# Performance work log

Measured on AMD Instinct MI355X. Metric: run time of the kernel, lower is better.

## Reference

```python
import jax, jax.numpy as jnp
import numpy as np

IN_F = 4096
OUT_F = 4096
N = 16384


def setup_inputs() -> dict:
    key = jax.random.key(0)
    kx, kw = jax.random.split(key)
    x = jax.random.normal(kx, (N, IN_F), dtype=jnp.float32)
    # reset_parameters: weight ~ N(0, 1/in_features), bias = 0
    weight = jax.random.normal(kw, (OUT_F, IN_F), dtype=jnp.float32) * (1.0 / np.sqrt(IN_F))
    bias = jnp.zeros((OUT_F,), dtype=jnp.float32)
    return {"x": x, "weight": weight, "bias": bias}


def reference(x, weight, bias):
    # binary_linear_scalar: per-output-row scaling factor alpha = mean(|W|),
    # binarized weight bw = sign(W) * alpha  (XNOR-Net style)
    alpha = jnp.mean(jnp.abs(weight), axis=1, keepdims=True)  # [out, 1]
    bw = jnp.sign(weight) * alpha                             # [out, in]
    # y = x @ bw^T + bias
    return jnp.einsum('ni,oi->no', x, bw) + bias
```

## Files before the change

### kernel.cpp

```cpp
#include <hip/hip_runtime.h>
#include <hip/hip_bf16.h>
#include <stdint.h>

#define IN_F  4096
#define OUT_F 4096
#define NROWS 16384
#define NT    (IN_F / 64)

typedef unsigned short u16;
typedef unsigned int u32;
typedef unsigned long long u64;
typedef __bf16 bf16x8 __attribute__((ext_vector_type(8)));
typedef float  f32x4  __attribute__((ext_vector_type(4)));
typedef u16    u16x8  __attribute__((ext_vector_type(8)));

#define BAR()   asm volatile("s_barrier" ::: "memory")
#define LGKM0() asm volatile("s_waitcnt lgkmcnt(0)" ::: "memory")
#define VM4()   asm volatile("s_waitcnt vmcnt(4)" ::: "memory")
#define VM0()   asm volatile("s_waitcnt vmcnt(0)" ::: "memory")

__device__ __forceinline__ u16 f2bf(float x) {
    union { float f; uint32_t u; } c; c.f = x;
    uint32_t u = c.u;
    return (u16)((u + 0x7FFFu + ((u >> 16) & 1u)) >> 16);
}

__device__ __forceinline__ void gload_lds16(const void* g, void* l) {
    __builtin_amdgcn_global_load_lds(
        (const __attribute__((address_space(1))) void*)g,
        (__attribute__((address_space(3))) void*)l, 16, 0, 0);
}

__device__ __forceinline__ u16 sgn_bf16(float v) {
    return v > 0.f ? 0x3F80 : (v < 0.f ? 0xBF80 : 0);
}

__global__ void prep_wbits_kernel(const float* __restrict__ W,
                                  float* __restrict__ alpha,
                                  u64* __restrict__ Wbits) {
    const int row = blockIdx.x;
    const int wave = threadIdx.x >> 6, lane = threadIdx.x & 63;
    const float* wr = W + (size_t)row * IN_F;
    float s = 0.f;
#pragma unroll 4
    for (int it = 0; it < 16; ++it) {
        const int kword = it * 4 + wave;
        float v = __builtin_nontemporal_load(wr + kword * 64 + lane);
        s += fabsf(v);
        u64 m = __ballot(v > 0.f);
        if (lane == 0) Wbits[(size_t)kword * OUT_F + row] = m;
    }
    for (int off = 32; off > 0; off >>= 1) s += __shfl_down(s, off);
    __shared__ float red[4];
    if (lane == 0) red[wave] = s;
    __syncthreads();
    if (threadIdx.x == 0)
        alpha[row] = (red[0] + red[1] + red[2] + red[3]) * (1.0f / IN_F);
}

__global__ void convx_kernel(const float* __restrict__ X, u16* __restrict__ O,
                             int swz) {
    const size_t idx = (size_t)blockIdx.x * 256 + threadIdx.x;
    const int row = (int)(idx >> 9);
    const int q = (int)idx & 511;
    const int g = q >> 3, c8 = q & 7;
    const int c8s = swz ? (c8 ^ (row & 7)) : c8;
    const f32x4* src = reinterpret_cast<const f32x4*>(
        X + (size_t)row * IN_F + g * 64 + c8s * 8);
    f32x4 a = __builtin_nontemporal_load(src);
    f32x4 b = __builtin_nontemporal_load(src + 1);
    u16x8 r;
    r[0] = f2bf(a[0]); r[1] = f2bf(a[1]); r[2] = f2bf(a[2]); r[3] = f2bf(a[3]);
    r[4] = f2bf(b[0]); r[5] = f2bf(b[1]); r[6] = f2bf(b[2]); r[7] = f2bf(b[3]);
    reinterpret_cast<u16x8*>(O)[idx] = r;
}

__global__ __launch_bounds__(512, 2) void gemm8_kernel(
    const u16* __restrict__ Xbf, const u64* __restrict__ Wbits,
    const float* __restrict__ alpha, const float* __restrict__ bias,
    float* __restrict__ Y) {
    __shared__ u16 Alds[3][16384];
    __shared__ u16 Blds[2][16384];

    const int tid  = threadIdx.x;
    const int lane = tid & 63, wave = tid >> 6;
    const int wm = wave >> 2, wn = wave & 3;
    const int lrow = lane & 15;

    const int wg = blockIdx.x;
    const int i  = wg >> 3;
    const int m0 = (((wg & 7) << 3) | (i >> 4)) << 8;
    const int n0 = (i & 15) << 8;

    const int q0 = ((lane >> 4) << 3) ^ ((lrow & 7) << 3);
    const int q1 = q0 ^ 32;

    const int erow = tid >> 1, ehalf = tid & 1;
    const u32* Wb32 = reinterpret_cast<const u32*>(Wbits);

    f32x4 acc[8][4];
#pragma unroll
    for (int a = 0; a < 8; ++a)
#pragma unroll
        for (int b = 0; b < 4; ++b) acc[a][b] = (f32x4){0.f, 0.f, 0.f, 0.f};

    auto stageA = [&](int th, int half, u16* buf) {
        if (th >= NT) return;
#pragma unroll
        for (int t2 = 0; t2 < 2; ++t2) {
            const int c = half * 1024 + t2 * 512 + tid;
            const int row = c >> 3, c8 = c & 7;
            gload_lds16(Xbf + (size_t)(m0 + row) * IN_F + th * 64 + c8 * 8,
                        buf + c * 8);
        }
    };

    auto expandB = [&](unsigned b, int dstbuf, int jlo) {
        unsigned nb = ~b;
        u16* base = &Blds[dstbuf][erow * 64];
#pragma unroll
        for (int j = 0; j < 2; ++j) {
            const int jj = jlo + j;
            const int k8 = 4 * ehalf + jj;
            union { unsigned u[4]; u16x8 v; } r;
#pragma unroll
            for (int e = 0; e < 4; ++e) {
                unsigned s = nb >> (jj * 8 + 2 * e);
                r.u[e] = 0x3F803F80u | ((s & 1u) << 15) | ((s & 2u) << 30);
            }
            *reinterpret_cast<u16x8*>(base + ((k8 ^ (erow & 7)) << 3)) = r.v;
        }
    };

    u16* pa0 = &Alds[0][0];
    u16* pa1 = &Alds[1][0];
    u16* pa2 = &Alds[2][0];

    unsigned b0 = Wb32[(size_t)(n0 + erow) * 2 + ehalf];
    stageA(0, 0, pa0); stageA(0, 1, pa0);
    unsigned bits_cur = Wb32[(size_t)8192 + (n0 + erow) * 2 + ehalf];
    stageA(1, 0, pa1); stageA(1, 1, pa1);
    unsigned bits_nxt = 0;
    expandB(b0, 0, 0); expandB(b0, 0, 2);
    VM4();
    LGKM0(); BAR();

    for (int t = 0; t < NT; ++t) {
        const u16* Ar = pa0 + wm * 8192 + lrow * 64;
        const u16* Br = &Blds[t & 1][0] + wn * 4096 + lrow * 64;
        bf16x8 a0[4][2], a1[4][2], bfr[4][2];

#pragma unroll
        for (int mm = 0; mm < 4; ++mm) {
            a0[mm][0] = *reinterpret_cast<const bf16x8*>(Ar + mm * 1024 + q0);
            a0[mm][1] = *reinterpret_cast<const bf16x8*>(Ar + mm * 1024 + q1);
        }
#pragma unroll
        for (int nf = 0; nf < 4; ++nf) {
            bfr[nf][0] = *reinterpret_cast<const bf16x8*>(Br + nf * 1024 + q0);
            bfr[nf][1] = *reinterpret_cast<const bf16x8*>(Br + nf * 1024 + q1);
        }
#pragma unroll
        for (int mm = 0; mm < 4; ++mm) {
            a1[mm][0] = *reinterpret_cast<const bf16x8*>(Ar + (4 + mm) * 1024 + q0);
            a1[mm][1] = *reinterpret_cast<const bf16x8*>(Ar + (4 + mm) * 1024 + q1);
        }
        if (t + 2 < NT)
            bits_nxt = Wb32[(size_t)(t + 2) * 8192 + (n0 + erow) * 2 + ehalf];

        __builtin_amdgcn_s_setprio(1);
#pragma unroll
        for (int mm = 0; mm < 4; ++mm)
#pragma unroll
            for (int nn = 0; nn < 4; ++nn) {
                acc[mm][nn] = __builtin_amdgcn_mfma_f32_16x16x32_bf16(a0[mm][0], bfr[nn][0], acc[mm][nn], 0, 0, 0);
                acc[mm][nn] = __builtin_amdgcn_mfma_f32_16x16x32_bf16(a0[mm][1], bfr[nn][1], acc[mm][nn], 0, 0, 0);
            }
        __builtin_amdgcn_s_setprio(0);

        stageA(t + 2, 0, pa2);
        stageA(t + 2, 1, pa2);
        if (t + 1 < NT) {
            expandB(bits_cur, (t + 1) & 1, 0);
            expandB(bits_cur, (t + 1) & 1, 2);
        }

        __builtin_amdgcn_s_setprio(1);
#pragma unroll
        for (int mm = 0; mm < 4; ++mm)
#pragma unroll
            for (int nn = 0; nn < 4; ++nn) {
                acc[4 + mm][nn] = __builtin_amdgcn_mfma_f32_16x16x32_bf16(a1[mm][0], bfr[nn][0], acc[4 + mm][nn], 0, 0, 0);
                acc[4 + mm][nn] = __builtin_amdgcn_mfma_f32_16x16x32_bf16(a1[mm][1], bfr[nn][1], acc[4 + mm][nn], 0, 0, 0);
            }
        __builtin_amdgcn_s_setprio(0);

        if (t >= NT - 2) { VM0(); } else { VM4(); }
        LGKM0(); BAR();

        bits_cur = bits_nxt;
        u16* tp = pa0; pa0 = pa1; pa1 = pa2; pa2 = tp;
    }

#pragma unroll
    for (int nf = 0; nf < 4; ++nf) {
        const int col = n0 + wn * 64 + nf * 16 + lrow;
        const float al = alpha[col], bi = bias[col];
#pragma unroll
        for (int mf = 0; mf < 8; ++mf) {
            const int rbase = m0 + wm * 128 + mf * 16 + ((lane >> 4) << 2);
#pragma unroll
            for (int r = 0; r < 4; ++r)
                __builtin_nontemporal_store(acc[mf][nf][r] * al + bi,
                    &Y[(size_t)(rbase + r) * OUT_F + col]);
        }
    }
}

__global__ void prep_w_kernel(const float* __restrict__ W,
                              float* __restrict__ alpha,
                              u16* __restrict__ S) {
    const int row = blockIdx.x;
    const float* wr = W + (size_t)row * IN_F;
    float s = 0.f;
    for (int c = threadIdx.x; c < 512; c += 256) {
        const f32x4* src = reinterpret_cast<const f32x4*>(wr + c * 8);
        f32x4 v0 = __builtin_nontemporal_load(src);
        f32x4 v1 = __builtin_nontemporal_load(src + 1);
        s += fabsf(v0[0]) + fabsf(v0[1]) + fabsf(v0[2]) + fabsf(v0[3])
           + fabsf(v1[0]) + fabsf(v1[1]) + fabsf(v1[2]) + fabsf(v1[3]);
        u16x8 r;
        r[0] = sgn_bf16(v0[0]); r[1] = sgn_bf16(v0[1]);
        r[2] = sgn_bf16(v0[2]); r[3] = sgn_bf16(v0[3]);
        r[4] = sgn_bf16(v1[0]); r[5] = sgn_bf16(v1[1]);
        r[6] = sgn_bf16(v1[2]); r[7] = sgn_bf16(v1[3]);
        *reinterpret_cast<u16x8*>(S + (size_t)row * IN_F + c * 8) = r;
    }
    for (int off = 32; off > 0; off >>= 1) s += __shfl_down(s, off);
    __shared__ float red[4];
    const int wave = threadIdx.x >> 6, lane = threadIdx.x & 63;
    if (lane == 0) red[wave] = s;
    __syncthreads();
    if (threadIdx.x == 0)
        alpha[row] = (red[0] + red[1] + red[2] + red[3]) * (1.0f / IN_F);
}

__global__ __launch_bounds__(256) void gemm_fallback(
    const float* __restrict__ X, const u16* __restrict__ Wsign,
    const float* __restrict__ alpha, const float* __restrict__ bias,
    float* __restrict__ Y) {
    __shared__ u16 Axl[128 * 64];
    __shared__ u16 Bxl[128 * 64];

    const int tid = threadIdx.x;
    const int n0 = blockIdx.x * 128;
    const int m0 = blockIdx.y * 128;
    const int wave = tid >> 6, lane = tid & 63;
    const int wm = wave >> 1, wn = wave & 1;
    const int lrow = lane & 15;
    const int lk8 = (lane >> 4) * 8;

    f32x4 acc[4][4];
#pragma unroll
    for (int a = 0; a < 4; ++a)
#pragma unroll
        for (int b = 0; b < 4; ++b) acc[a][b] = (f32x4){0.f, 0.f, 0.f, 0.f};

    for (int kt = 0; kt < IN_F; kt += 64) {
#pragma unroll
        for (int j = 0; j < 4; ++j) {
            const int idx = j * 256 + tid;
            const int row = idx >> 3, c8 = idx & 7;
            gload_lds16(Wsign + (size_t)(n0 + row) * IN_F + kt + c8 * 8,
                        &Bxl[idx * 8]);
        }
#pragma unroll
        for (int j = 0; j < 4; ++j) {
            const int idx = j * 256 + tid;
            const int row = idx >> 3, c8 = idx & 7;
            const float* src = X + (size_t)(m0 + row) * IN_F + kt + c8 * 8;
            float4 v0 = *reinterpret_cast<const float4*>(src);
            float4 v1 = *reinterpret_cast<const float4*>(src + 4);
            u16x8 r;
            r[0] = f2bf(v0.x); r[1] = f2bf(v0.y); r[2] = f2bf(v0.z); r[3] = f2bf(v0.w);
            r[4] = f2bf(v1.x); r[5] = f2bf(v1.y); r[6] = f2bf(v1.z); r[7] = f2bf(v1.w);
            *reinterpret_cast<u16x8*>(&Axl[idx * 8]) = r;
        }
        __syncthreads();
#pragma unroll
        for (int kk = 0; kk < 2; ++kk) {
            bf16x8 af[4], bfv[4];
#pragma unroll
            for (int mf = 0; mf < 4; ++mf)
                af[mf] = *reinterpret_cast<const bf16x8*>(
                    &Axl[(wm * 64 + mf * 16 + lrow) * 64 + kk * 32 + lk8]);
#pragma unroll
            for (int nf = 0; nf < 4; ++nf)
                bfv[nf] = *reinterpret_cast<const bf16x8*>(
                    &Bxl[(wn * 64 + nf * 16 + lrow) * 64 + kk * 32 + lk8]);
#pragma unroll
            for (int mf = 0; mf < 4; ++mf)
#pragma unroll
                for (int nf = 0; nf < 4; ++nf)
                    acc[mf][nf] = __builtin_amdgcn_mfma_f32_16x16x32_bf16(
                        af[mf], bfv[nf], acc[mf][nf], 0, 0, 0);
        }
        __syncthreads();
    }
#pragma unroll
    for (int nf = 0; nf < 4; ++nf) {
        const int col = n0 + wn * 64 + nf * 16 + lrow;
        const float al = alpha[col], bi = bias[col];
#pragma unroll
        for (int mf = 0; mf < 4; ++mf) {
            const int rbase = m0 + wm * 64 + mf * 16 + (lane >> 4) * 4;
#pragma unroll
            for (int r = 0; r < 4; ++r)
                __builtin_nontemporal_store(acc[mf][nf][r] * al + bi,
                    &Y[(size_t)(rbase + r) * OUT_F + col]);
        }
    }
}

extern "C" void kernel_launch(void* const* d_in, const int* in_sizes, int n_in,
                              void* d_out, int out_size, void* d_ws, size_t ws_size,
                              hipStream_t stream) {
    const float* X    = (const float*)d_in[0];
    const float* W    = (const float*)d_in[1];
    const float* bias = (const float*)d_in[2];
    float* Y = (float*)d_out;

    char* ws = (char*)d_ws;
    float* alpha = (float*)ws;
    const size_t WBITS_OFF = 16384;
    const size_t XBF_OFF   = WBITS_OFF + (size_t)OUT_F * (IN_F / 8);
    const size_t need_fast = XBF_OFF + (size_t)NROWS * IN_F * 2;

    if (ws_size >= need_fast) {
        u64* Wbits = (u64*)(ws + WBITS_OFF);
        u16* Xbf   = (u16*)(ws + XBF_OFF);
        prep_wbits_kernel<<<OUT_F, 256, 0, stream>>>(W, alpha, Wbits);
        convx_kernel<<<(size_t)NROWS * IN_F / 8 / 256, 256, 0, stream>>>(X, Xbf, 1);
        gemm8_kernel<<<dim3(1024), 512, 0, stream>>>(Xbf, Wbits, alpha, bias, Y);
    } else {
        u16* Wsign = (u16*)(ws + 16384);
        prep_w_kernel<<<OUT_F, 256, 0, stream>>>(W, alpha, Wsign);
        dim3 grid(OUT_F / 128, NROWS / 128);
        gemm_fallback<<<grid, 256, 0, stream>>>(X, Wsign, alpha, bias, Y);
    }
}
```

Baseline: 523.5 us.

## Software-pipeline A fragment LDS loads and interleave staging with MFMA blocks

Result: no change. 514.3 us (-1.8%).

```diff
diff --git a/kernel.cpp b/kernel.cpp
--- a/kernel.cpp
+++ b/kernel.cpp
@@ -148,52 +148,39 @@
     for (int t = 0; t < NT; ++t) {
         const u16* Ar = pa0 + wm * 8192 + lrow * 64;
         const u16* Br = &Blds[t & 1][0] + wn * 4096 + lrow * 64;
-        bf16x8 a0[4][2], a1[4][2], bfr[4][2];
-
-#pragma unroll
-        for (int mm = 0; mm < 4; ++mm) {
-            a0[mm][0] = *reinterpret_cast<const bf16x8*>(Ar + mm * 1024 + q0);
-            a0[mm][1] = *reinterpret_cast<const bf16x8*>(Ar + mm * 1024 + q1);
-        }
+        bf16x8 bfr[4][2];
+
 #pragma unroll
         for (int nf = 0; nf < 4; ++nf) {
             bfr[nf][0] = *reinterpret_cast<const bf16x8*>(Br + nf * 1024 + q0);
             bfr[nf][1] = *reinterpret_cast<const bf16x8*>(Br + nf * 1024 + q1);
         }
-#pragma unroll
-        for (int mm = 0; mm < 4; ++mm) {
-            a1[mm][0] = *reinterpret_cast<const bf16x8*>(Ar + (4 + mm) * 1024 + q0);
-            a1[mm][1] = *reinterpret_cast<const bf16x8*>(Ar + (4 + mm) * 1024 + q1);
-        }
         if (t + 2 < NT)
             bits_nxt = Wb32[(size_t)(t + 2) * 8192 + (n0 + erow) * 2 + ehalf];
 
-        __builtin_amdgcn_s_setprio(1);
-#pragma unroll
-        for (int mm = 0; mm < 4; ++mm)
+        bf16x8 aP0 = *reinterpret_cast<const bf16x8*>(Ar + q0);
+        bf16x8 aP1 = *reinterpret_cast<const bf16x8*>(Ar + q1);
+#pragma unroll
+        for (int mm = 0; mm < 8; ++mm) {
+            bf16x8 aQ0, aQ1;
+            if (mm < 7) {
+                aQ0 = *reinterpret_cast<const bf16x8*>(Ar + (mm + 1) * 1024 + q0);
+                aQ1 = *reinterpret_cast<const bf16x8*>(Ar + (mm + 1) * 1024 + q1);
+            }
+            if (mm == 1) stageA(t + 2, 0, pa2);
+            if (mm == 3 && t + 1 < NT) expandB(bits_cur, (t + 1) & 1, 0);
+            if (mm == 4) stageA(t + 2, 1, pa2);
+            if (mm == 5 && t + 1 < NT) expandB(bits_cur, (t + 1) & 1, 2);
+
+            __builtin_amdgcn_s_setprio(1);
 #pragma unroll
             for (int nn = 0; nn < 4; ++nn) {
-                acc[mm][nn] = __builtin_amdgcn_mfma_f32_16x16x32_bf16(a0[mm][0], bfr[nn][0], acc[mm][nn], 0, 0, 0);
-                acc[mm][nn] = __builtin_amdgcn_mfma_f32_16x16x32_bf16(a0[mm][1], bfr[nn][1], acc[mm][nn], 0, 0, 0);
+                acc[mm][nn] = __builtin_amdgcn_mfma_f32_16x16x32_bf16(aP0, bfr[nn][0], acc[mm][nn], 0, 0, 0);
+                acc[mm][nn] = __builtin_amdgcn_mfma_f32_16x16x32_bf16(aP1, bfr[nn][1], acc[mm][nn], 0, 0, 0);
             }
-        __builtin_amdgcn_s_setprio(0);
-
-        stageA(t + 2, 0, pa2);
-        stageA(t + 2, 1, pa2);
-        if (t + 1 < NT) {
-            expandB(bits_cur, (t + 1) & 1, 0);
-            expandB(bits_cur, (t + 1) & 1, 2);
-        }
-
-        __builtin_amdgcn_s_setprio(1);
-#pragma unroll
-        for (int mm = 0; mm < 4; ++mm)
-#pragma unroll
-            for (int nn = 0; nn < 4; ++nn) {
-                acc[4 + mm][nn] = __builtin_amdgcn_mfma_f32_16x16x32_bf16(a1[mm][0], bfr[nn][0], acc[4 + mm][nn], 0, 0, 0);
-                acc[4 + mm][nn] = __builtin_amdgcn_mfma_f32_16x16x32_bf16(a1[mm][1], bfr[nn][1], acc[4 + mm][nn], 0, 0, 0);
-            }
-        __builtin_amdgcn_s_setprio(0);
+            __builtin_amdgcn_s_setprio(0);
+            aP0 = aQ0; aP1 = aQ1;
+        }
 
         if (t >= NT - 2) { VM0(); } else { VM4(); }
         LGKM0(); BAR();
```
